# Kernel optimization log

Hardware: AMD Instinct MI355X
Metric: run time of the kernel (lower is better)

The kernel has to match this reference:

```python
import jax, jax.numpy as jnp
import numpy as np
import math

N_HEADS = 12


def setup_inputs() -> dict:
    key = jax.random.key(0)
    ks = jax.random.split(key, 6)
    B, S, DIM = 4, 2048, 768
    h = jax.random.normal(ks[0], (B, S, DIM), dtype=jnp.float32)
    attn_mask = jnp.ones((B, 1, 1, S), dtype=jnp.int32)
    scale = 1.0 / math.sqrt(DIM)
    wq = jax.random.normal(ks[1], (DIM, DIM), dtype=jnp.float32) * scale
    wk = jax.random.normal(ks[2], (DIM, DIM), dtype=jnp.float32) * scale
    wv = jax.random.normal(ks[3], (DIM, DIM), dtype=jnp.float32) * scale
    wo = jax.random.normal(ks[4], (DIM, DIM), dtype=jnp.float32) * scale
    return {"h": h, "attn_mask": attn_mask, "wq": wq, "wk": wk, "wv": wv, "wo": wo}


def reference(h, attn_mask, wq, wk, wv, wo):
    B, S, dim = h.shape
    H = N_HEADS
    D = dim // H
    qk_scale = 1.0 / math.sqrt(D)
    # NOTE: original uses .view(B, H, S, D) on the [B, S, H*D] projection —
    # a raw reshape, NOT the usual (B,S,H,D)->(B,H,S,D) transpose. Reproduce exactly.
    hq = (h @ wq.T).reshape(B, H, S, D)
    hk = (h @ wk.T).reshape(B, H, S, D)
    hv = (h @ wv.T).reshape(B, H, S, D)
    scores = jnp.einsum("bhqd,bhkd->bhqk", hq, hk) * qk_scale  # [B,H,S,S]
    scores = jnp.where(attn_mask == 0, -jnp.inf, scores)
    attn = jax.nn.softmax(scores.astype(jnp.float32), axis=-1)
    ctx = jnp.einsum("bhqk,bhkd->bhqd", attn, hv)  # [B,H,S,D]
    # dropout is identity in eval mode
    ctx = ctx.reshape(B, S, H * D)
    return ctx @ wo.T
```

## Files before the change

kernel.cpp:

```cpp
#include <hip/hip_runtime.h>
#include <math.h>

typedef __bf16 bf16x8 __attribute__((ext_vector_type(8)));
typedef float  f32x4  __attribute__((ext_vector_type(4)));
typedef float  f32x16 __attribute__((ext_vector_type(16)));

#define MFMA16(a, b, c) __builtin_amdgcn_mfma_f32_16x16x32_bf16((a), (b), (c), 0, 0, 0)
#define MFMA32(a, b, c) __builtin_amdgcn_mfma_f32_32x32x16_bf16((a), (b), (c), 0, 0, 0)

__device__ __forceinline__ unsigned short f2bf(float f) {
    unsigned int u = __float_as_uint(f);
    u += 0x7fffu + ((u >> 16) & 1u);
    return (unsigned short)(u >> 16);
}

__device__ __forceinline__ void gll16(const unsigned short* g, unsigned short* l) {
    __builtin_amdgcn_global_load_lds(
        (const __attribute__((address_space(1))) unsigned int*)g,
        (__attribute__((address_space(3))) unsigned int*)l, 16, 0, 0);
}

__global__ __launch_bounds__(256) void convert_kernel(
    const float* __restrict__ h, const float* __restrict__ wq,
    const float* __restrict__ wk, const float* __restrict__ wv,
    const float* __restrict__ wo,
    unsigned short* __restrict__ hb, unsigned short* __restrict__ wb)
{
    const int NH4 = 1572864;
    const int NW4 = 147456;
    int i4 = blockIdx.x * 256 + threadIdx.x;
    const float4* src;
    unsigned short* dst;
    int off;
    float sc = 1.0f;
    if (i4 < NH4) {
        src = (const float4*)h; dst = hb; off = i4;
    } else {
        int j = i4 - NH4;
        int w = j / NW4;
        off = j - w * NW4;
        const float* s = (w == 0) ? wq : (w == 1) ? wk : (w == 2) ? wv : wo;
        if (w == 0) sc = 0.18033688011112042f;
        src = (const float4*)s;
        dst = wb + w * 589824;
    }
    float4 v = src[off];
    ushort4 o;
    o.x = f2bf(v.x * sc); o.y = f2bf(v.y * sc);
    o.z = f2bf(v.z * sc); o.w = f2bf(v.w * sc);
    ((ushort4*)dst)[off] = o;
}

template <typename OutT>
__global__ __launch_bounds__(256) void gemm_bt(
    const unsigned short* __restrict__ A,
    const unsigned short* __restrict__ Bm,
    OutT* __restrict__ C)
{
    constexpr int K = 768, N = 768;
    __shared__ unsigned short As[3][128 * 32];
    __shared__ unsigned short Bs[3][128 * 32];

    const int nwg  = gridDim.x;
    const int orig = blockIdx.x;
    const int lid  = (orig & 7) * (nwg >> 3) + (orig >> 3);
    const int ncol = nwg >> 6;
    const int cix  = lid % ncol;
    const int bm   = (lid / ncol) * 128;
    const int nx   = cix % 6;
    const int bz   = cix / 6;
    const int bn   = nx * 128;

    const unsigned short* Bz = Bm + (size_t)bz * N * K;
    OutT* Cz = C + (size_t)bz * 8192 * N;

    const int tid  = threadIdx.x;
    const int wave = tid >> 6, lane = tid & 63;
    const int wm   = (wave & 1) * 64, wn = (wave >> 1) * 64;
    const int l16  = lane & 15, quad = lane >> 4;

    const int sr  = tid >> 2;
    const int sp8 = ((tid & 3) ^ (sr & 3)) * 8;
    const int slot8 = (quad ^ (l16 & 3)) * 8;

    auto stage = [&](int k0, int bi) {
        gll16(A  + (size_t)(bm + sr) * K      + k0 + sp8, As[bi] + tid * 8);
        gll16(A  + (size_t)(bm + 64 + sr) * K + k0 + sp8, As[bi] + 2048 + tid * 8);
        gll16(Bz + (size_t)(bn + sr) * K      + k0 + sp8, Bs[bi] + tid * 8);
        gll16(Bz + (size_t)(bn + 64 + sr) * K + k0 + sp8, Bs[bi] + 2048 + tid * 8);
    };

    f32x4 acc[4][4] = {};

    stage(0, 0);
    stage(32, 1);

    int cur = 0;
    for (int i = 0; i < 24; i++) {
        if (i < 23) asm volatile("s_waitcnt vmcnt(4)\n\ts_barrier" ::: "memory");
        else        asm volatile("s_waitcnt vmcnt(0)\n\ts_barrier" ::: "memory");
        __builtin_amdgcn_sched_barrier(0);

        if (i < 22) {
            int nb = cur + 2; if (nb >= 3) nb -= 3;
            stage((i + 2) * 32, nb);
        }

        bf16x8 af[4], bfv[4];
        #pragma unroll
        for (int ii = 0; ii < 4; ii++)
            af[ii] = *(const bf16x8*)(As[cur] + (wm + ii * 16 + l16) * 32 + slot8);
        #pragma unroll
        for (int jj = 0; jj < 4; jj++)
            bfv[jj] = *(const bf16x8*)(Bs[cur] + (wn + jj * 16 + l16) * 32 + slot8);
        #pragma unroll
        for (int ii = 0; ii < 4; ii++)
            #pragma unroll
            for (int jj = 0; jj < 4; jj++)
                acc[ii][jj] = MFMA16(af[ii], bfv[jj], acc[ii][jj]);

        cur = (cur == 2) ? 0 : cur + 1;
    }

    #pragma unroll
    for (int ii = 0; ii < 4; ii++) {
        #pragma unroll
        for (int jj = 0; jj < 4; jj++) {
            int row0 = bm + wm + ii * 16 + quad * 4;
            int col  = bn + wn + jj * 16 + l16;
            #pragma unroll
            for (int r = 0; r < 4; r++) {
                float v = acc[ii][jj][r];
                size_t idx = (size_t)(row0 + r) * N + col;
                if constexpr (sizeof(OutT) == 2) Cz[idx] = f2bf(v);
                else                             Cz[idx] = v;
            }
        }
    }
}

__global__ __launch_bounds__(256) void vtrans_kernel(
    const unsigned short* __restrict__ Vg,
    unsigned short* __restrict__ vt)
{
    constexpr int LDT = 72;
    __shared__ unsigned short Ts[64 * LDT];
    const int b = blockIdx.z, hh = blockIdx.y, kp0 = blockIdx.x * 64;
    const int tid = threadIdx.x;
    const size_t boff = (size_t)b * (24576 * 64);
    const int rowV0 = hh * 2048 + kp0;

    #pragma unroll
    for (int rep = 0; rep < 2; rep++) {
        int idx = rep * 256 + tid;
        int r = idx >> 3, dp = (idx & 7) * 8;
        uint4 v = *(const uint4*)(Vg + boff + (size_t)(rowV0 + r) * 64 + dp);
        unsigned short tmp[8];
        *(uint4*)tmp = v;
        #pragma unroll
        for (int i = 0; i < 8; i++) Ts[(dp + i) * LDT + r] = tmp[i];
    }
    __syncthreads();
    unsigned short* vtb = vt + ((size_t)(b * 12 + hh)) * 64 * 2048;
    #pragma unroll
    for (int rep = 0; rep < 2; rep++) {
        int idx = rep * 256 + tid;
        int d = idx >> 3, kp = (idx & 7) * 8;
        uint4 v = *(const uint4*)(Ts + d * LDT + kp);
        *(uint4*)(vtb + (size_t)d * 2048 + kp0 + kp) = v;
    }
}

__global__ __launch_bounds__(256) void attn_kernel(
    const unsigned short* __restrict__ Qg,
    const unsigned short* __restrict__ Kg,
    const unsigned short* __restrict__ vt,
    const int* __restrict__ mask,
    unsigned short* __restrict__ Og)
{
    __shared__ unsigned short Ks[3 * 2048];
    __shared__ unsigned short Vs[3 * 2048];
    __shared__ unsigned long long msh[32];

    const int orig = blockIdx.x;
    const int lid  = (orig & 7) * 96 + (orig >> 3);
    const int qt   = lid & 15;
    const int bh   = lid >> 4;
    const int hh   = bh % 12;
    const int b    = bh / 12;

    const int tid  = threadIdx.x;
    const int wave = tid >> 6, lane = tid & 63;
    const int c31  = lane & 31, h = lane >> 5;
    const size_t boff = (size_t)b * (24576 * 64);
    const int rowQ0 = hh * 2048 + qt * 128;
    const int rowK0 = hh * 2048;
    const unsigned short* vtg = vt + ((size_t)(b * 12 + hh)) * 64 * 2048;
    const int swk = (c31 & 7) ^ (c31 >> 3);
    const int swv = (c31 & 3) ^ ((c31 >> 2) & 3);

    const int srowK = tid >> 3;
    const int schK  = ((tid & 7) ^ (srowK & 7) ^ ((srowK >> 3) & 3)) * 8;
    const int srowV = tid >> 2;
    const int schV  = ((tid & 3) ^ (srowV & 3) ^ ((srowV >> 2) & 3)) * 8;

    auto stageKV = [&](int kt, int bi) {
        gll16(Kg  + boff + (size_t)(rowK0 + kt * 32 + srowK) * 64 + schK,
              Ks + bi * 2048 + tid * 8);
        gll16(vtg + (size_t)srowV * 2048 + kt * 32 + schV,
              Vs + bi * 2048 + tid * 8);
    };

    bf16x8 qf[4];
    {
        const unsigned short* qrow =
            Qg + boff + (size_t)(rowQ0 + wave * 32 + c31) * 64;
        #pragma unroll
        for (int c = 0; c < 4; c++)
            qf[c] = *(const bf16x8*)(qrow + (2 * c + h) * 8);
    }

    {
        const int4 a = *(const int4*)(mask + b * 2048 + tid * 8);
        const int4 c = *(const int4*)(mask + b * 2048 + tid * 8 + 4);
        unsigned char byte =
            (a.x != 0 ? 1u : 0u)       | (a.y != 0 ? 2u : 0u) |
            (a.z != 0 ? 4u : 0u)       | (a.w != 0 ? 8u : 0u) |
            (c.x != 0 ? 16u : 0u)      | (c.y != 0 ? 32u : 0u) |
            (c.z != 0 ? 64u : 0u)      | (c.w != 0 ? 128u : 0u);
        ((unsigned char*)msh)[tid] = byte;
    }
    __syncthreads();

    stageKV(0, 0);
    stageKV(1, 1);

    f32x16 acc[2] = {};
    f32x16 acc_l  = {};
    bf16x8 onesf;
    #pragma unroll
    for (int i = 0; i < 8; i++) onesf[i] = (__bf16)1.0f;

    int cur = 0;
    for (int kt = 0; kt < 64; kt++) {
        if (kt < 63) asm volatile("s_waitcnt vmcnt(2)\n\ts_barrier" ::: "memory");
        else         asm volatile("s_waitcnt vmcnt(0)\n\ts_barrier" ::: "memory");
        __builtin_amdgcn_sched_barrier(0);

        if (kt < 62) {
            int nb = cur + 2; if (nb >= 3) nb -= 3;
            stageKV(kt + 2, nb);
        }

        const unsigned int am = ((const unsigned int*)msh)[kt];
        const unsigned short* Kc = Ks + cur * 2048;
        const unsigned short* Vc = Vs + cur * 2048;

        f32x16 sT;
        {
            f32x16 z2 = {};
            __builtin_amdgcn_s_setprio(1);
            #pragma unroll
            for (int c = 0; c < 4; c++) {
                int ch = (2 * c + h) ^ swk;
                bf16x8 kf = *(const bf16x8*)(Kc + c31 * 64 + ch * 8);
                z2 = MFMA32(kf, qf[c], z2);
            }
            __builtin_amdgcn_s_setprio(0);
            sT = z2;
        }

        unsigned int p01[4], p23[4];
        if (am == 0xFFFFFFFFu) {
            #pragma unroll
            for (int s = 0; s < 4; s++) {
                float e0 = __builtin_amdgcn_exp2f(sT[4*s+0]);
                float e1 = __builtin_amdgcn_exp2f(sT[4*s+1]);
                float e2 = __builtin_amdgcn_exp2f(sT[4*s+2]);
                float e3 = __builtin_amdgcn_exp2f(sT[4*s+3]);
                asm("v_cvt_pk_bf16_f32 %0, %1, %2"
                    : "=v"(p01[s]) : "v"(e0), "v"(e1));
                asm("v_cvt_pk_bf16_f32 %0, %1, %2"
                    : "=v"(p23[s]) : "v"(e2), "v"(e3));
            }
        } else {
            #pragma unroll
            for (int s = 0; s < 4; s++) {
                unsigned int nib = (am >> (8 * s + 4 * h)) & 0xFu;
                float e0 = __builtin_amdgcn_exp2f(sT[4*s+0]);
                float e1 = __builtin_amdgcn_exp2f(sT[4*s+1]);
                float e2 = __builtin_amdgcn_exp2f(sT[4*s+2]);
                float e3 = __builtin_amdgcn_exp2f(sT[4*s+3]);
                e0 = (nib & 1u) ? e0 : 0.f;
                e1 = (nib & 2u) ? e1 : 0.f;
                e2 = (nib & 4u) ? e2 : 0.f;
                e3 = (nib & 8u) ? e3 : 0.f;
                asm("v_cvt_pk_bf16_f32 %0, %1, %2"
                    : "=v"(p01[s]) : "v"(e0), "v"(e1));
                asm("v_cvt_pk_bf16_f32 %0, %1, %2"
                    : "=v"(p23[s]) : "v"(e2), "v"(e3));
            }
        }

        __builtin_amdgcn_s_setprio(1);
        #pragma unroll
        for (int kc = 0; kc < 2; kc++) {
            unsigned int a01 = p01[2 * kc], b01 = p01[2 * kc + 1];
            unsigned int a23 = p23[2 * kc], b23 = p23[2 * kc + 1];
            asm("v_permlane32_swap_b32 %0, %1" : "+v"(a01), "+v"(b01));
            asm("v_permlane32_swap_b32 %0, %1" : "+v"(a23), "+v"(b23));
            uint4 pfu;
            pfu.x = a01;
            pfu.y = a23;
            pfu.z = b01;
            pfu.w = b23;
            bf16x8 pf;
            __builtin_memcpy(&pf, &pfu, 16);
            #pragma unroll
            for (int nt = 0; nt < 2; nt++) {
                int chv = (2 * kc + h) ^ swv;
                bf16x8 vf = *(const bf16x8*)(Vc + (nt * 32 + c31) * 32 + chv * 8);
                acc[nt] = MFMA32(pf, vf, acc[nt]);
            }
            acc_l = MFMA32(pf, onesf, acc_l);
        }
        __builtin_amdgcn_s_setprio(0);

        cur = (cur == 2) ? 0 : cur + 1;
    }

    #pragma unroll
    for (int reg = 0; reg < 16; reg++) {
        int rowfn = (reg & 3) + 8 * (reg >> 2) + 4 * h;
        float li = __builtin_amdgcn_rcpf(acc_l[reg]);
        int row = rowQ0 + wave * 32 + rowfn;
        #pragma unroll
        for (int nt = 0; nt < 2; nt++)
            Og[boff + (size_t)row * 64 + nt * 32 + c31] = f2bf(acc[nt][reg] * li);
    }
}

extern "C" void kernel_launch(void* const* d_in, const int* in_sizes, int n_in,
                              void* d_out, int out_size, void* d_ws, size_t ws_size,
                              hipStream_t stream)
{
    const float* h    = (const float*)d_in[0];
    const int*   mask = (const int*)d_in[1];
    const float* wq   = (const float*)d_in[2];
    const float* wk   = (const float*)d_in[3];
    const float* wv   = (const float*)d_in[4];
    const float* wo   = (const float*)d_in[5];

    unsigned short* hb  = (unsigned short*)d_ws;
    unsigned short* wb  = hb + 6291456;
    unsigned short* qkv = wb + 4 * 589824;
    unsigned short* ctx = qkv + (size_t)3 * 6291456;

    convert_kernel<<<8448, 256, 0, stream>>>(h, wq, wk, wv, wo, hb, wb);
    gemm_bt<unsigned short><<<1152, 256, 0, stream>>>(hb, wb, qkv);
    vtrans_kernel<<<dim3(32, 12, 4), 256, 0, stream>>>(
        qkv + (size_t)2 * 6291456, hb);
    attn_kernel<<<768, 256, 0, stream>>>(
        qkv, qkv + 6291456, hb, mask, ctx);
    gemm_bt<float><<<384, 256, 0, stream>>>(
        ctx, wb + (size_t)3 * 589824, (float*)d_out);
}
```

Baseline: 232.1 us.

## Process two KV tiles per attention iteration and halve output GEMM M-tile

The attention loop now handles two 32-key tiles per barrier with a 6-deep LDS ring, prefetching two tiles ahead. This halves the number of barriers and waits and gives the scheduler more independent MFMA and exp work to interleave. Separately, the output projection GEMM is templated on BM and launched with 64-row tiles, doubling its grid from 384 to 768 blocks to fill the CUs better. In exchange, attention LDS use doubles, which may reduce occupancy, and the mask fast path now requires both tiles to be fully unmasked.

```diff
diff --git a/kernel.cpp b/kernel.cpp
--- a/kernel.cpp
+++ b/kernel.cpp
@@ -51,22 +51,24 @@
     ((ushort4*)dst)[off] = o;
 }
 
-template <typename OutT>
+template <typename OutT, int BM>
 __global__ __launch_bounds__(256) void gemm_bt(
     const unsigned short* __restrict__ A,
     const unsigned short* __restrict__ Bm,
     OutT* __restrict__ C)
 {
     constexpr int K = 768, N = 768;
-    __shared__ unsigned short As[3][128 * 32];
+    constexpr int MI = BM / 32;
+    constexpr int NDMA = (BM == 128) ? 4 : 3;
+    __shared__ unsigned short As[3][BM * 32];
     __shared__ unsigned short Bs[3][128 * 32];
 
     const int nwg  = gridDim.x;
     const int orig = blockIdx.x;
     const int lid  = (orig & 7) * (nwg >> 3) + (orig >> 3);
-    const int ncol = nwg >> 6;
+    const int ncol = (nwg * BM) >> 13;
     const int cix  = lid % ncol;
-    const int bm   = (lid / ncol) * 128;
+    const int bm   = (lid / ncol) * BM;
     const int nx   = cix % 6;
     const int bz   = cix / 6;
     const int bn   = nx * 128;
@@ -76,7 +78,7 @@
 
     const int tid  = threadIdx.x;
     const int wave = tid >> 6, lane = tid & 63;
-    const int wm   = (wave & 1) * 64, wn = (wave >> 1) * 64;
+    const int wm   = (wave & 1) * (BM / 2), wn = (wave >> 1) * 64;
     const int l16  = lane & 15, quad = lane >> 4;
 
     const int sr  = tid >> 2;
@@ -85,20 +87,25 @@
 
     auto stage = [&](int k0, int bi) {
         gll16(A  + (size_t)(bm + sr) * K      + k0 + sp8, As[bi] + tid * 8);
-        gll16(A  + (size_t)(bm + 64 + sr) * K + k0 + sp8, As[bi] + 2048 + tid * 8);
+        if (BM == 128)
+            gll16(A + (size_t)(bm + 64 + sr) * K + k0 + sp8, As[bi] + 2048 + tid * 8);
         gll16(Bz + (size_t)(bn + sr) * K      + k0 + sp8, Bs[bi] + tid * 8);
         gll16(Bz + (size_t)(bn + 64 + sr) * K + k0 + sp8, Bs[bi] + 2048 + tid * 8);
     };
 
-    f32x4 acc[4][4] = {};
+    f32x4 acc[MI][4] = {};
 
     stage(0, 0);
     stage(32, 1);
 
     int cur = 0;
     for (int i = 0; i < 24; i++) {
-        if (i < 23) asm volatile("s_waitcnt vmcnt(4)\n\ts_barrier" ::: "memory");
-        else        asm volatile("s_waitcnt vmcnt(0)\n\ts_barrier" ::: "memory");
+        if (i < 23) {
+            if (BM == 128) asm volatile("s_waitcnt vmcnt(4)\n\ts_barrier" ::: "memory");
+            else           asm volatile("s_waitcnt vmcnt(3)\n\ts_barrier" ::: "memory");
+        } else {
+            asm volatile("s_waitcnt vmcnt(0)\n\ts_barrier" ::: "memory");
+        }
         __builtin_amdgcn_sched_barrier(0);
 
         if (i < 22) {
@@ -106,15 +113,15 @@
             stage((i + 2) * 32, nb);
         }
 
-        bf16x8 af[4], bfv[4];
-        #pragma unroll
-        for (int ii = 0; ii < 4; ii++)
+        bf16x8 af[MI], bfv[4];
+        #pragma unroll
+        for (int ii = 0; ii < MI; ii++)
             af[ii] = *(const bf16x8*)(As[cur] + (wm + ii * 16 + l16) * 32 + slot8);
         #pragma unroll
         for (int jj = 0; jj < 4; jj++)
             bfv[jj] = *(const bf16x8*)(Bs[cur] + (wn + jj * 16 + l16) * 32 + slot8);
         #pragma unroll
-        for (int ii = 0; ii < 4; ii++)
+        for (int ii = 0; ii < MI; ii++)
             #pragma unroll
             for (int jj = 0; jj < 4; jj++)
                 acc[ii][jj] = MFMA16(af[ii], bfv[jj], acc[ii][jj]);
@@ -123,7 +130,7 @@
     }
 
     #pragma unroll
-    for (int ii = 0; ii < 4; ii++) {
+    for (int ii = 0; ii < MI; ii++) {
         #pragma unroll
         for (int jj = 0; jj < 4; jj++) {
             int row0 = bm + wm + ii * 16 + quad * 4;
@@ -178,8 +185,8 @@
     const int* __restrict__ mask,
     unsigned short* __restrict__ Og)
 {
-    __shared__ unsigned short Ks[3 * 2048];
-    __shared__ unsigned short Vs[3 * 2048];
+    __shared__ unsigned short Ks[6 * 2048];
+    __shared__ unsigned short Vs[6 * 2048];
     __shared__ unsigned long long msh[32];
 
     const int orig = blockIdx.x;
@@ -234,6 +241,8 @@
 
     stageKV(0, 0);
     stageKV(1, 1);
+    stageKV(2, 2);
+    stageKV(3, 3);
 
     f32x16 acc[2] = {};
     f32x16 acc_l  = {};
@@ -242,91 +251,153 @@
     for (int i = 0; i < 8; i++) onesf[i] = (__bf16)1.0f;
 
     int cur = 0;
-    for (int kt = 0; kt < 64; kt++) {
-        if (kt < 63) asm volatile("s_waitcnt vmcnt(2)\n\ts_barrier" ::: "memory");
-        else         asm volatile("s_waitcnt vmcnt(0)\n\ts_barrier" ::: "memory");
+    for (int j = 0; j < 32; j++) {
+        if (j < 31) asm volatile("s_waitcnt vmcnt(4)\n\ts_barrier" ::: "memory");
+        else        asm volatile("s_waitcnt vmcnt(0)\n\ts_barrier" ::: "memory");
         __builtin_amdgcn_sched_barrier(0);
 
-        if (kt < 62) {
-            int nb = cur + 2; if (nb >= 3) nb -= 3;
-            stageKV(kt + 2, nb);
-        }
-
-        const unsigned int am = ((const unsigned int*)msh)[kt];
-        const unsigned short* Kc = Ks + cur * 2048;
-        const unsigned short* Vc = Vs + cur * 2048;
-
-        f32x16 sT;
+        if (j < 30) {
+            int nb0 = cur + 4; if (nb0 >= 6) nb0 -= 6;
+            int nb1 = cur + 5; if (nb1 >= 6) nb1 -= 6;
+            stageKV(2 * j + 4, nb0);
+            stageKV(2 * j + 5, nb1);
+        }
+
+        const int c1 = (cur == 5) ? 0 : cur + 1;
+        const unsigned int am0 = ((const unsigned int*)msh)[2 * j];
+        const unsigned int am1 = ((const unsigned int*)msh)[2 * j + 1];
+        const unsigned short* Kc0 = Ks + cur * 2048;
+        const unsigned short* Vc0 = Vs + cur * 2048;
+        const unsigned short* Kc1 = Ks + c1 * 2048;
+        const unsigned short* Vc1 = Vs + c1 * 2048;
+        const bool full = (am0 & am1) == 0xFFFFFFFFu;
+
+        unsigned int a01[4], a23[4];
         {
             f32x16 z2 = {};
             __builtin_amdgcn_s_setprio(1);
             #pragma unroll
             for (int c = 0; c < 4; c++) {
                 int ch = (2 * c + h) ^ swk;
-                bf16x8 kf = *(const bf16x8*)(Kc + c31 * 64 + ch * 8);
+                bf16x8 kf = *(const bf16x8*)(Kc0 + c31 * 64 + ch * 8);
                 z2 = MFMA32(kf, qf[c], z2);
             }
             __builtin_amdgcn_s_setprio(0);
-            sT = z2;
-        }
-
-        unsigned int p01[4], p23[4];
-        if (am == 0xFFFFFFFFu) {
-            #pragma unroll
-            for (int s = 0; s < 4; s++) {
-                float e0 = __builtin_amdgcn_exp2f(sT[4*s+0]);
-                float e1 = __builtin_amdgcn_exp2f(sT[4*s+1]);
-                float e2 = __builtin_amdgcn_exp2f(sT[4*s+2]);
-                float e3 = __builtin_amdgcn_exp2f(sT[4*s+3]);
-                asm("v_cvt_pk_bf16_f32 %0, %1, %2"
-                    : "=v"(p01[s]) : "v"(e0), "v"(e1));
-                asm("v_cvt_pk_bf16_f32 %0, %1, %2"
-                    : "=v"(p23[s]) : "v"(e2), "v"(e3));
-            }
-        } else {
-            #pragma unroll
-            for (int s = 0; s < 4; s++) {
-                unsigned int nib = (am >> (8 * s + 4 * h)) & 0xFu;
-                float e0 = __builtin_amdgcn_exp2f(sT[4*s+0]);
-                float e1 = __builtin_amdgcn_exp2f(sT[4*s+1]);
-                float e2 = __builtin_amdgcn_exp2f(sT[4*s+2]);
-                float e3 = __builtin_amdgcn_exp2f(sT[4*s+3]);
-                e0 = (nib & 1u) ? e0 : 0.f;
-                e1 = (nib & 2u) ? e1 : 0.f;
-                e2 = (nib & 4u) ? e2 : 0.f;
-                e3 = (nib & 8u) ? e3 : 0.f;
-                asm("v_cvt_pk_bf16_f32 %0, %1, %2"
-                    : "=v"(p01[s]) : "v"(e0), "v"(e1));
-                asm("v_cvt_pk_bf16_f32 %0, %1, %2"
-                    : "=v"(p23[s]) : "v"(e2), "v"(e3));
+            if (full) {
+                #pragma unroll
+                for (int s = 0; s < 4; s++) {
+                    float e0 = __builtin_amdgcn_exp2f(z2[4*s+0]);
+                    float e1 = __builtin_amdgcn_exp2f(z2[4*s+1]);
+                    float e2 = __builtin_amdgcn_exp2f(z2[4*s+2]);
+                    float e3 = __builtin_amdgcn_exp2f(z2[4*s+3]);
+                    asm("v_cvt_pk_bf16_f32 %0, %1, %2"
+                        : "=v"(a01[s]) : "v"(e0), "v"(e1));
+                    asm("v_cvt_pk_bf16_f32 %0, %1, %2"
+                        : "=v"(a23[s]) : "v"(e2), "v"(e3));
+                }
+            } else {
+                #pragma unroll
+                for (int s = 0; s < 4; s++) {
+                    unsigned int nib = (am0 >> (8 * s + 4 * h)) & 0xFu;
+                    float e0 = __builtin_amdgcn_exp2f(z2[4*s+0]);
+                    float e1 = __builtin_amdgcn_exp2f(z2[4*s+1]);
+                    float e2 = __builtin_amdgcn_exp2f(z2[4*s+2]);
+                    float e3 = __builtin_amdgcn_exp2f(z2[4*s+3]);
+                    e0 = (nib & 1u) ? e0 : 0.f;
+                    e1 = (nib & 2u) ? e1 : 0.f;
+                    e2 = (nib & 4u) ? e2 : 0.f;
+                    e3 = (nib & 8u) ? e3 : 0.f;
+                    asm("v_cvt_pk_bf16_f32 %0, %1, %2"
+                        : "=v"(a01[s]) : "v"(e0), "v"(e1));
+                    asm("v_cvt_pk_bf16_f32 %0, %1, %2"
+                        : "=v"(a23[s]) : "v"(e2), "v"(e3));
+                }
+            }
+        }
+
+        unsigned int b01[4], b23[4];
+        {
+            f32x16 z2 = {};
+            __builtin_amdgcn_s_setprio(1);
+            #pragma unroll
+            for (int c = 0; c < 4; c++) {
+                int ch = (2 * c + h) ^ swk;
+                bf16x8 kf = *(const bf16x8*)(Kc1 + c31 * 64 + ch * 8);
+                z2 = MFMA32(kf, qf[c], z2);
+            }
+            __builtin_amdgcn_s_setprio(0);
+            if (full) {
+                #pragma unroll
+                for (int s = 0; s < 4; s++) {
+                    float e0 = __builtin_amdgcn_exp2f(z2[4*s+0]);
+                    float e1 = __builtin_amdgcn_exp2f(z2[4*s+1]);
+                    float e2 = __builtin_amdgcn_exp2f(z2[4*s+2]);
+                    float e3 = __builtin_amdgcn_exp2f(z2[4*s+3]);
+                    asm("v_cvt_pk_bf16_f32 %0, %1, %2"
+                        : "=v"(b01[s]) : "v"(e0), "v"(e1));
+                    asm("v_cvt_pk_bf16_f32 %0, %1, %2"
+                        : "=v"(b23[s]) : "v"(e2), "v"(e3));
+                }
+            } else {
+                #pragma unroll
+                for (int s = 0; s < 4; s++) {
+                    unsigned int nib = (am1 >> (8 * s + 4 * h)) & 0xFu;
+                    float e0 = __builtin_amdgcn_exp2f(z2[4*s+0]);
+                    float e1 = __builtin_amdgcn_exp2f(z2[4*s+1]);
+                    float e2 = __builtin_amdgcn_exp2f(z2[4*s+2]);
+                    float e3 = __builtin_amdgcn_exp2f(z2[4*s+3]);
+                    e0 = (nib & 1u) ? e0 : 0.f;
+                    e1 = (nib & 2u) ? e1 : 0.f;
+                    e2 = (nib & 4u) ? e2 : 0.f;
+                    e3 = (nib & 8u) ? e3 : 0.f;
+                    asm("v_cvt_pk_bf16_f32 %0, %1, %2"
+                        : "=v"(b01[s]) : "v"(e0), "v"(e1));
+                    asm("v_cvt_pk_bf16_f32 %0, %1, %2"
+                        : "=v"(b23[s]) : "v"(e2), "v"(e3));
+                }
             }
         }
 
         __builtin_amdgcn_s_setprio(1);
         #pragma unroll
         for (int kc = 0; kc < 2; kc++) {
-            unsigned int a01 = p01[2 * kc], b01 = p01[2 * kc + 1];
-            unsigned int a23 = p23[2 * kc], b23 = p23[2 * kc + 1];
-            asm("v_permlane32_swap_b32 %0, %1" : "+v"(a01), "+v"(b01));
-            asm("v_permlane32_swap_b32 %0, %1" : "+v"(a23), "+v"(b23));
+            unsigned int x01 = a01[2 * kc], y01 = a01[2 * kc + 1];
+            unsigned int x23 = a23[2 * kc], y23 = a23[2 * kc + 1];
+            asm("v_permlane32_swap_b32 %0, %1" : "+v"(x01), "+v"(y01));
+            asm("v_permlane32_swap_b32 %0, %1" : "+v"(x23), "+v"(y23));
             uint4 pfu;
-            pfu.x = a01;
-            pfu.y = a23;
-            pfu.z = b01;
-            pfu.w = b23;
+            pfu.x = x01; pfu.y = x23; pfu.z = y01; pfu.w = y23;
             bf16x8 pf;
             __builtin_memcpy(&pf, &pfu, 16);
             #pragma unroll
             for (int nt = 0; nt < 2; nt++) {
                 int chv = (2 * kc + h) ^ swv;
-                bf16x8 vf = *(const bf16x8*)(Vc + (nt * 32 + c31) * 32 + chv * 8);
+                bf16x8 vf = *(const bf16x8*)(Vc0 + (nt * 32 + c31) * 32 + chv * 8);
                 acc[nt] = MFMA32(pf, vf, acc[nt]);
             }
             acc_l = MFMA32(pf, onesf, acc_l);
         }
+        #pragma unroll
+        for (int kc = 0; kc < 2; kc++) {
+            unsigned int x01 = b01[2 * kc], y01 = b01[2 * kc + 1];
+            unsigned int x23 = b23[2 * kc], y23 = b23[2 * kc + 1];
+            asm("v_permlane32_swap_b32 %0, %1" : "+v"(x01), "+v"(y01));
+            asm("v_permlane32_swap_b32 %0, %1" : "+v"(x23), "+v"(y23));
+            uint4 pfu;
+            pfu.x = x01; pfu.y = x23; pfu.z = y01; pfu.w = y23;
+            bf16x8 pf;
+            __builtin_memcpy(&pf, &pfu, 16);
+            #pragma unroll
+            for (int nt = 0; nt < 2; nt++) {
+                int chv = (2 * kc + h) ^ swv;
+                bf16x8 vf = *(const bf16x8*)(Vc1 + (nt * 32 + c31) * 32 + chv * 8);
+                acc[nt] = MFMA32(pf, vf, acc[nt]);
+            }
+            acc_l = MFMA32(pf, onesf, acc_l);
+        }
         __builtin_amdgcn_s_setprio(0);
 
-        cur = (cur == 2) ? 0 : cur + 1;
+        cur = (cur >= 4) ? cur - 4 : cur + 2;
     }
 
     #pragma unroll
@@ -357,11 +428,11 @@
     unsigned short* ctx = qkv + (size_t)3 * 6291456;
 
     convert_kernel<<<8448, 256, 0, stream>>>(h, wq, wk, wv, wo, hb, wb);
-    gemm_bt<unsigned short><<<1152, 256, 0, stream>>>(hb, wb, qkv);
+    gemm_bt<unsigned short, 128><<<1152, 256, 0, stream>>>(hb, wb, qkv);
     vtrans_kernel<<<dim3(32, 12, 4), 256, 0, stream>>>(
         qkv + (size_t)2 * 6291456, hb);
     attn_kernel<<<768, 256, 0, stream>>>(
         qkv, qkv + 6291456, hb, mask, ctx);
-    gemm_bt<float><<<384, 256, 0, stream>>>(
+    gemm_bt<float, 64><<<768, 256, 0, stream>>>(
         ctx, wb + (size_t)3 * 589824, (float*)d_out);
 }
```

After: 229.1 us. Within noise of the previous version (-1.3%).
